# Kernel optimization log

Hardware: AMD Instinct MI355X
Metric: run time of the kernel (lower is better)

Reference implementation:

```python
import jax, jax.numpy as jnp
import numpy as np
import math

DIM = 384
HEADS = 6
HID = 32  # PositionalEncodingFourier hidden_dim
B, H, W = 16, 56, 56


def _layer_norm(x, g, b, eps=1e-6):
    mu = jnp.mean(x, axis=-1, keepdims=True)
    var = jnp.mean((x - mu) ** 2, axis=-1, keepdims=True)
    return (x - mu) * jax.lax.rsqrt(var + eps) * g + b


def _pos_encoding_fourier(Bb, Hh, Ww, w, b):
    # EdgeNeXt PositionalEncodingFourier with all-False mask: cumsum == arange+1
    scale = 2.0 * math.pi
    y_embed = jnp.arange(1, Hh + 1, dtype=jnp.float32)[:, None] / (Hh + 1e-6) * scale
    x_embed = jnp.arange(1, Ww + 1, dtype=jnp.float32)[None, :] / (Ww + 1e-6) * scale
    dim_t = 10000.0 ** (2.0 * (jnp.arange(HID) // 2).astype(jnp.float32) / HID)
    def enc(e):
        p = jnp.broadcast_to(e, (Hh, Ww))[..., None] / dim_t  # (H,W,HID)
        return jnp.stack([jnp.sin(p[..., 0::2]), jnp.cos(p[..., 1::2])], axis=-1).reshape(Hh, Ww, HID)
    pos = jnp.concatenate([enc(y_embed), enc(x_embed)], axis=-1)  # (H,W,2*HID)
    pos = pos @ w.T + b  # 1x1 conv token_projection as matmul -> (H,W,DIM)
    return jnp.broadcast_to(jnp.transpose(pos, (2, 0, 1))[None], (Bb, DIM, Hh, Ww))


def _forward(x, pos_w, pos_b, ln_g, ln_b, gamma_xca, temperature,
             qkv_w, qkv_b, proj_w, proj_b, rpb_table, conv_w,
             bn_g, bn_b, bn_mean, bn_var, gamma):
    Bb, C, Hh, Ww = x.shape
    N = Hh * Ww
    d = C // HEADS
    xt = jnp.transpose(x.reshape(Bb, C, N), (0, 2, 1))  # (B,N,C)
    pos = _pos_encoding_fourier(Bb, Hh, Ww, pos_w, pos_b)
    xt = xt + jnp.transpose(pos.reshape(Bb, C, N), (0, 2, 1))

    # relative position bias (seq_len T=2): gather (T,T,h) -> expand (h,d^2,T,T)
    # -> nearest interp x0.5 selects element (0,0) -> pixel_shuffle(d) of constant
    # channels == per-head scalar broadcast over the (d,d) channel-attention map.
    T = 2
    rel_idx = jnp.arange(T)[:, None] - jnp.arange(T)[None, :] + T - 1  # (2,2)
    rpb = rpb_table[rel_idx.reshape(-1)].reshape(T, T, HEADS)
    bias = rpb[0, 0][None, :, None, None]  # (1,heads,1,1), broadcasts over (d,d)

    # XCA: cross-covariance (channel) attention
    xn = _layer_norm(xt, ln_g, ln_b)
    qkv = (xn @ qkv_w.T + qkv_b).reshape(Bb, N, 3, HEADS, d)
    qkv = jnp.transpose(qkv, (2, 0, 3, 4, 1))  # (3,B,h,d,N)
    q, k, v = qkv[0], qkv[1], qkv[2]
    q = q / jnp.maximum(jnp.linalg.norm(q, axis=-1, keepdims=True), 1e-12)
    k = k / jnp.maximum(jnp.linalg.norm(k, axis=-1, keepdims=True), 1e-12)
    attn = jnp.einsum('bhdn,bhen->bhde', q, k) * temperature + bias  # (B,h,d,d)
    attn = jax.nn.softmax(attn, axis=-1)
    out = jnp.einsum('bhde,bhen->bhdn', attn, v)  # (B,h,d,N)
    out = jnp.transpose(out, (0, 3, 1, 2)).reshape(Bb, N, C)
    out = out @ proj_w.T + proj_b
    xt = xt + gamma_xca * out

    x2 = jnp.transpose(xt, (0, 2, 1)).reshape(Bb, C, Hh, Ww)
    # pwconv0: conv3x3 (dim->dim, expan_ration hardcoded to 1) + BN(inference) + SiLU
    xi = jax.lax.conv_general_dilated(x2, conv_w, (1, 1), [(1, 1), (1, 1)],
                                      dimension_numbers=('NCHW', 'OIHW', 'NCHW'))
    xi = (xi - bn_mean[None, :, None, None]) * jax.lax.rsqrt(bn_var + 1e-5)[None, :, None, None]
    xi = xi * bn_g[None, :, None, None] + bn_b[None, :, None, None]
    xi = xi * jax.nn.sigmoid(xi)  # SiLU
    x2 = x2 + xi

    # faithful to source: raw reshape (NOT permute) of contiguous NCHW into (B,H,W,C)
    x3 = x2.reshape(Bb, Hh, Ww, C) * gamma
    x3 = jnp.transpose(x3, (0, 3, 1, 2))
    return x + x3


def setup_inputs() -> dict:
    key = jax.random.key(0)
    ks = jax.random.split(key, 10)
    d3 = 3 * DIM
    return {
        'x': jax.random.normal(ks[0], (B, DIM, H, W), jnp.float32),
        'pos_w': jax.random.normal(ks[1], (DIM, 2 * HID), jnp.float32) * 0.05,
        'pos_b': jnp.zeros((DIM,), jnp.float32),
        'ln_g': jnp.ones((DIM,), jnp.float32),
        'ln_b': jnp.zeros((DIM,), jnp.float32),
        'gamma_xca': jax.random.normal(ks[2], (DIM,), jnp.float32) * 0.1,
        'temperature': jnp.ones((HEADS, 1, 1), jnp.float32),
        'qkv_w': jax.random.normal(ks[3], (d3, DIM), jnp.float32) * (DIM ** -0.5),
        'qkv_b': jnp.zeros((d3,), jnp.float32),
        'proj_w': jax.random.normal(ks[4], (DIM, DIM), jnp.float32) * (DIM ** -0.5),
        'proj_b': jnp.zeros((DIM,), jnp.float32),
        'rpb_table': jax.random.normal(ks[5], (3, HEADS), jnp.float32) * 0.02,
        'conv_w': jax.random.normal(ks[6], (DIM, DIM, 3, 3), jnp.float32) * 0.02,
        'bn_g': jnp.ones((DIM,), jnp.float32),
        'bn_b': jnp.zeros((DIM,), jnp.float32),
        'bn_mean': jax.random.normal(ks[7], (DIM,), jnp.float32) * 0.1,
        'bn_var': jax.random.uniform(ks[8], (DIM,), jnp.float32, 0.5, 1.5),
        'gamma': jax.random.normal(ks[9], (DIM,), jnp.float32) * 0.1,
    }


def reference(x, pos_w, pos_b, ln_g, ln_b, gamma_xca, temperature,
              qkv_w, qkv_b, proj_w, proj_b, rpb_table, conv_w,
              bn_g, bn_b, bn_mean, bn_var, gamma):
    return _forward(x, pos_w, pos_b, ln_g, ln_b, gamma_xca, temperature,
                    qkv_w, qkv_b, proj_w, proj_b, rpb_table, conv_w,
                    bn_g, bn_b, bn_mean, bn_var, gamma)
```

## Files before the change

### kernel.cpp

```cpp
#include <hip/hip_runtime.h>
#include <hip/hip_bf16.h>
#include <math.h>

#define DIM 384
#define HEADS 6
#define NN 3136
#define BB 16
#define BH (BB*HEADS)
#define HP 58
#define NP (HP*HP)

typedef __attribute__((ext_vector_type(8))) short short8;
typedef __attribute__((ext_vector_type(4))) short short4v;
typedef __attribute__((ext_vector_type(4))) float f32x4;

__device__ __forceinline__ float bf2f(unsigned short u) {
    union { unsigned int i; float f; } v; v.i = ((unsigned int)u) << 16; return v.f;
}
__device__ __forceinline__ unsigned short f2bf(float f) {
    union { float f; unsigned int i; } v; v.f = f;
    unsigned int r = v.i + 0x7fffu + ((v.i >> 16) & 1u);
    return (unsigned short)(r >> 16);
}
__device__ __forceinline__ void glds16(const unsigned short* g, void* l) {
    __builtin_amdgcn_global_load_lds(
        (const __attribute__((address_space(1))) unsigned int*)g,
        (__attribute__((address_space(3))) unsigned int*)l, 16, 0, 0);
}

__global__ void kw_convert(const float* __restrict__ qkv_w, const float* __restrict__ proj_w,
                           const float* __restrict__ conv_w,
                           unsigned short* __restrict__ Wq, unsigned short* __restrict__ Wp,
                           unsigned short* __restrict__ Wc) {
    int tid = blockIdx.x * 256 + threadIdx.x;
    int stride = gridDim.x * 256;
    for (int i = tid; i < 3*DIM*DIM; i += stride) Wq[i] = f2bf(qkv_w[i]);
    for (int i = tid; i < DIM*DIM; i += stride) Wp[i] = f2bf(proj_w[i]);
    for (int i = tid; i < DIM*DIM*9; i += stride) {
        int ii = i % DIM; int rest = i / DIM; int tap = rest % 9; int o = rest / 9;
        Wc[i] = f2bf(conv_w[(size_t)(o*DIM + ii)*9 + tap]);
    }
}

__global__ void k_pos(const float* __restrict__ pos_w, const float* __restrict__ pos_b,
                      float* __restrict__ P) {
    int n = blockIdx.x; int h = n / 56, w = n % 56;
    __shared__ float feat[64];
    int t = threadIdx.x;
    if (t < 64) {
        int axis = t >> 5;
        int k = t & 31; int i = k >> 1;
        float e = (float)((axis ? w : h) + 1) / 56.000001f * 6.28318530717958647692f;
        float arg = e / powf(10000.0f, (float)i / 16.0f);
        feat[t] = (k & 1) ? cosf(arg) : sinf(arg);
    }
    __syncthreads();
    for (int c = t; c < DIM; c += blockDim.x) {
        float s = pos_b[c];
        #pragma unroll 8
        for (int k = 0; k < 64; k++) s += feat[k] * pos_w[c*64 + k];
        P[(size_t)n*DIM + c] = s;
    }
}

__global__ __launch_bounds__(256) void k_tln(const float* __restrict__ x, const float* __restrict__ P,
                                             const float* __restrict__ g, const float* __restrict__ be,
                                             unsigned short* __restrict__ XTb, unsigned short* __restrict__ XN) {
    __shared__ float tile[32][388];
    int blk = blockIdx.x;
    int b = blk / 98, nt = blk % 98;
    int n0 = nt*32;
    int t = threadIdx.x;
    #pragma unroll
    for (int it = 0; it < 12; it++) {
        int task = it*256 + t;
        int c = task >> 3, seg = task & 7;
        float4 v = *reinterpret_cast<const float4*>(x + ((size_t)(b*DIM + c))*NN + n0 + seg*4);
        tile[seg*4+0][c] = v.x; tile[seg*4+1][c] = v.y;
        tile[seg*4+2][c] = v.z; tile[seg*4+3][c] = v.w;
    }
    __syncthreads();
    int row = t >> 3, sub = t & 7;
    int n = n0 + row;
    f32x4 xp[12];
    float s = 0.f;
    #pragma unroll
    for (int k = 0; k < 12; k++) {
        int c0 = (k*8 + sub)*4;
        float4 tv = *reinterpret_cast<float4*>(&tile[row][c0]);
        float4 pv = *reinterpret_cast<const float4*>(P + (size_t)n*DIM + c0);
        f32x4 xv = {tv.x+pv.x, tv.y+pv.y, tv.z+pv.z, tv.w+pv.w};
        xp[k] = xv;
        s += xv[0]+xv[1]+xv[2]+xv[3];
        unsigned short pkx[4];
        #pragma unroll
        for (int e=0;e<4;e++) pkx[e] = f2bf(xv[e]);
        *reinterpret_cast<short4v*>(XTb + ((size_t)(b*NN + n))*DIM + c0) = *(short4v*)pkx;
    }
    s += __shfl_xor(s, 1, 64); s += __shfl_xor(s, 2, 64); s += __shfl_xor(s, 4, 64);
    float mean = s * (1.0f/384.0f);
    float sq = 0.f;
    #pragma unroll
    for (int k = 0; k < 12; k++) {
        #pragma unroll
        for (int e = 0; e < 4; e++) { float d = xp[k][e]-mean; sq += d*d; }
    }
    sq += __shfl_xor(sq, 1, 64); sq += __shfl_xor(sq, 2, 64); sq += __shfl_xor(sq, 4, 64);
    float rs = rsqrtf(sq * (1.0f/384.0f) + 1e-6f);
    #pragma unroll
    for (int k = 0; k < 12; k++) {
        int c0 = (k*8 + sub)*4;
        unsigned short pk[4];
        #pragma unroll
        for (int e = 0; e < 4; e++)
            pk[e] = f2bf((xp[k][e]-mean)*rs*g[c0+e] + be[c0+e]);
        *reinterpret_cast<short4v*>(XN + ((size_t)(b*NN + n))*DIM + c0) = *(short4v*)pk;
    }
}

template<int MODE>
__global__ __launch_bounds__(256) void k_gemm(
    const unsigned short* __restrict__ A, const unsigned short* __restrict__ Wt,
    const float* __restrict__ bias,
    unsigned short* __restrict__ Qb, unsigned short* __restrict__ Kb, unsigned short* __restrict__ Vt,
    const unsigned short* __restrict__ XTb, const float* __restrict__ gxca, unsigned short* __restrict__ X2p)
{
    __shared__ __align__(16) char smem[35328];
    auto ctA = (float(*)[69])smem;
    auto ctB = (float(*)[130])smem;

    constexpr int NCT = (MODE == 0) ? 9 : 3;
    constexpr int CPX = (MODE == 0) ? 441 : 147;
    int bid = blockIdx.x;
    int orig = (bid & 7)*CPX + (bid >> 3);
    int ct = orig % NCT, mt = orig / NCT;
    int m0 = mt*128, o0 = ct*128;
    int t = threadIdx.x;
    int wave = t >> 6, lane = t & 63;
    int wr = wave >> 1, wc = wave & 1;
    int lr = lane & 15, lg = lane >> 4;

    int r0 = t >> 2;
    int swcol = (((t & 3) ^ ((t >> 3) & 3)) << 3);
    const unsigned short* a0 = A  + (size_t)(m0 + r0)*384 + swcol;
    const unsigned short* a1 = A  + (size_t)(m0 + 64 + r0)*384 + swcol;
    const unsigned short* b0 = Wt + (size_t)(o0 + r0)*384 + swcol;
    const unsigned short* b1 = Wt + (size_t)(o0 + 64 + r0)*384 + swcol;
    int rsw = ((lr >> 1) & 3) << 3;

    auto stage = [&](char* base, int c) {
        glds16(a0 + c, base + wave*1024);
        glds16(a1 + c, base + 4096 + wave*1024);
        glds16(b0 + c, base + 8192 + wave*1024);
        glds16(b1 + c, base + 12288 + wave*1024);
    };

    f32x4 acc[4][4];
    #pragma unroll
    for (int i=0;i<4;i++) for (int j=0;j<4;j++) acc[i][j] = (f32x4){0.f,0.f,0.f,0.f};

    stage(smem, 0);
    for (int kk = 0; kk < 12; kk++) {
        if (kk < 11) {
            stage(smem + ((kk+1)&1)*16384, (kk+1)*32);
            asm volatile("s_waitcnt vmcnt(4)" ::: "memory");
        } else {
            asm volatile("s_waitcnt vmcnt(0)" ::: "memory");
        }
        __builtin_amdgcn_s_barrier();
        __builtin_amdgcn_sched_barrier(0);
        auto As = (unsigned short(*)[32])(smem + (kk&1)*16384);
        auto Bs = (unsigned short(*)[32])(smem + (kk&1)*16384 + 8192);
        short8 af[4], bfv[4];
        #pragma unroll
        for (int i=0;i<4;i++) af[i]  = *(short8*)&As[wr*64 + i*16 + lr][(lg*8) ^ rsw];
        #pragma unroll
        for (int j=0;j<4;j++) bfv[j] = *(short8*)&Bs[wc*64 + j*16 + lr][(lg*8) ^ rsw];
        #pragma unroll
        for (int i=0;i<4;i++)
            #pragma unroll
            for (int j=0;j<4;j++)
                acc[i][j] = __builtin_amdgcn_mfma_f32_16x16x32_bf16(af[i], bfv[j], acc[i][j], 0, 0, 0);
        __builtin_amdgcn_s_barrier();
        __builtin_amdgcn_sched_barrier(0);
    }

    int comp = (MODE == 0) ? (o0 / DIM) : 0;
    for (int mh = 0; mh < 2; mh++) {
        __syncthreads();
        bool useB = (MODE == 1) || (MODE == 0 && comp == 2);
        if (wr == mh) {
            if (useB) {
                #pragma unroll
                for (int i=0;i<4;i++) for (int j=0;j<4;j++) for (int r=0;r<4;r++)
                    ctB[i*16 + lg*4 + r][wc*64 + j*16 + lr] = acc[i][j][r];
            } else {
                #pragma unroll
                for (int i=0;i<4;i++) for (int j=0;j<4;j++) for (int r=0;r<4;r++)
                    ctA[wc*64 + j*16 + lr][i*16 + lg*4 + r] = acc[i][j][r];
            }
        }
        __syncthreads();
        if (MODE == 1) {
            for (int q = t; q < 1024; q += 256) {
                int row = q >> 4, seg = q & 15;
                int m = m0 + mh*64 + row; int b = m/NN; int n = m - b*NN;
                int py = n/56, px = n - py*56;
                int og0 = o0 + seg*8;
                short8 xvb = *(const short8*)(XTb + (size_t)m*DIM + og0);
                unsigned short pk[8];
                #pragma unroll
                for (int e=0;e<8;e++) {
                    float val = ctB[row][seg*8+e] + bias[og0+e];
                    pk[e] = f2bf(bf2f((unsigned short)xvb[e]) + gxca[og0+e]*val);
                }
                *(short8*)(X2p + ((size_t)(b*NP + (py+1)*HP + px + 1))*DIM + og0) = *(short8*)pk;
            }
        } else if (comp < 2) {
            unsigned short* Dst = (comp == 0) ? Qb : Kb;
            for (int q = t; q < 2048; q += 256) {
                int row = q >> 4, seg = q & 15;
                int og = o0 + row; int rem = og - comp*DIM;
                int hh = rem >> 6, dd = rem & 63;
                int m4 = m0 + mh*64 + seg*4; int b = m4/NN; int n = m4 - b*NN;
                float bv = bias[og];
                unsigned short pk[4];
                #pragma unroll
                for (int e=0;e<4;e++) pk[e] = f2bf(ctA[row][seg*4+e] + bv);
                *(short4v*)(Dst + ((size_t)((b*HEADS + hh)*64 + dd))*NN + n) = *(short4v*)pk;
            }
        } else {
            for (int q = t; q < 1024; q += 256) {
                int row = q >> 4, seg = q & 15;
                int m = m0 + mh*64 + row; int b = m/NN; int n = m - b*NN;
                int og0 = o0 + seg*8; int rem0 = og0 - 2*DIM;
                int hh = rem0 >> 6, dd0 = rem0 & 63;
                unsigned short pk[8];
                #pragma unroll
                for (int e=0;e<8;e++) pk[e] = f2bf(ctB[row][seg*8+e] + bias[og0+e]);
                *(short8*)(Vt + ((size_t)((b*HEADS + hh)*NN + n))*64 + dd0) = *(short8*)pk;
            }
        }
    }
}

__global__ __launch_bounds__(256) void k_pad(unsigned short* __restrict__ X2p) {
    int b = blockIdx.x, part = blockIdx.y;
    unsigned short* base = X2p + (size_t)b*NP*DIM;
    short8 z = {0,0,0,0,0,0,0,0};
    for (int task = part*256 + threadIdx.x; task < 10944; task += 2048) {
        int pos = task / 48, seg = task - pos*48;
        int py, px;
        if (pos < 58)       { py = 0;  px = pos; }
        else if (pos < 116) { py = 57; px = pos - 58; }
        else if (pos < 172) { py = pos - 115; px = 0; }
        else                { py = pos - 171; px = 57; }
        *(short8*)(base + ((size_t)(py*HP + px))*DIM + seg*8) = z;
    }
}

__global__ __launch_bounds__(256, 3) void k_conv(
    const unsigned short* __restrict__ A, const unsigned short* __restrict__ Wt,
    const float* __restrict__ bn_g, const float* __restrict__ bn_b,
    const float* __restrict__ bn_mean, const float* __restrict__ bn_var,
    unsigned short* __restrict__ Yout)
{
    __shared__ __align__(16) char smem[49152];
    auto ctA = (float(*)[69])smem;
    auto X2s = (unsigned short(*)[68])(smem + 17664);

    int bid = blockIdx.x;
    int orig = (bid & 7)*150 + (bid >> 3);
    int ct = orig % 3; int rest = orig / 3;
    int tile = rest % 25; int b = rest / 25;
    int n0 = tile*128, o0 = ct*128;
    int t = threadIdx.x;
    int wave = t >> 6, lane = t & 63;
    int wr = wave >> 1, wc = wave & 1;
    int lr = lane & 15, lg = lane >> 4;
    int qb = n0 + 2*(n0/56);
    const size_t bbase = (size_t)b*NP*DIM;

    int swcol = (((t & 3) ^ ((t >> 3) & 3)) << 3);
    const unsigned short* asrc[4];
    #pragma unroll
    for (int j=0;j<4;j++) {
        int task = j*256 + t;
        int row = task >> 2;
        int q = qb + row; if (q > NP-1) q = NP-1;
        asrc[j] = A + bbase + (size_t)q*DIM + swcol;
    }
    const unsigned short* bsrc0 = Wt + (size_t)(o0 + (t>>2))*3456 + swcol;
    const unsigned short* bsrc1 = Wt + (size_t)(o0 + 64 + (t>>2))*3456 + swcol;

    int qrel[4];
    #pragma unroll
    for (int i=0;i<4;i++) {
        int loc = wr*64 + i*16 + lr;
        int n = n0 + loc; if (n >= NN) n = NN-1;
        qrel[i] = n + 2*(n/56) - qb;
    }

    auto stageA = [&](int bufsel, int c) {
        #pragma unroll
        for (int j=0;j<4;j++) glds16(asrc[j] + c, smem + bufsel*16384 + j*4096 + wave*1024);
    };
    auto stageB = [&](int slot, int off) {
        glds16(bsrc0 + off, smem + 32768 + slot*8192 + wave*1024);
        glds16(bsrc1 + off, smem + 32768 + slot*8192 + 4096 + wave*1024);
    };

    f32x4 acc[4][4];
    #pragma unroll
    for (int i=0;i<4;i++) for (int j=0;j<4;j++) acc[i][j] = (f32x4){0.f,0.f,0.f,0.f};

    stageA(0, 0); stageB(0, 0);
    for (int kk = 0; kk < 12; kk++) {
        auto Ah = (unsigned short(*)[32])(smem + (kk&1)*16384);
        #pragma unroll
        for (int tap = 0; tap < 9; tap++) {
            if (kk < 11 || tap < 8) {
                int off = (tap < 8) ? ((tap+1)*384 + kk*32) : ((kk+1)*32);
                stageB((kk+tap+1)&1, off);
            }
            if (tap == 6 && kk < 11) stageA((kk+1)&1, (kk+1)*32);
            if (kk < 11 && (tap == 6 || tap == 7))
                asm volatile("s_waitcnt vmcnt(6)" ::: "memory");
            else if (kk == 11 && tap == 8)
                asm volatile("s_waitcnt vmcnt(0)" ::: "memory");
            else
                asm volatile("s_waitcnt vmcnt(2)" ::: "memory");
            __builtin_amdgcn_s_barrier();
            __builtin_amdgcn_sched_barrier(0);
            auto Bs = (unsigned short(*)[32])(smem + 32768 + ((kk+tap)&1)*8192);
            int toff = (tap/3)*58 + (tap%3);
            short8 af[4], bfv[4];
            #pragma unroll
            for (int j=0;j<4;j++) {
                int brow = wc*64 + j*16 + lr;
                bfv[j] = *(short8*)&Bs[brow][(lg*8) ^ (((brow>>1)&3)<<3)];
            }
            #pragma unroll
            for (int i=0;i<4;i++) {
                int row = qrel[i] + toff;
                af[i] = *(short8*)&Ah[row][(lg*8) ^ (((row>>1)&3)<<3)];
            }
            #pragma unroll
            for (int i=0;i<4;i++)
                #pragma unroll
                for (int j=0;j<4;j++)
                    acc[i][j] = __builtin_amdgcn_mfma_f32_16x16x32_bf16(af[i], bfv[j], acc[i][j], 0, 0, 0);
            __builtin_amdgcn_s_barrier();
            __builtin_amdgcn_sched_barrier(0);
        }
    }

    for (int mh = 0; mh < 2; mh++) {
        for (int oh = 0; oh < 2; oh++) {
            __syncthreads();
            if (wr == mh && wc == oh) {
                #pragma unroll
                for (int i=0;i<4;i++) for (int j=0;j<4;j++) for (int r=0;r<4;r++)
                    ctA[j*16 + lr][i*16 + lg*4 + r] = acc[i][j][r];
            }
            for (int q = t; q < 512; q += 256) {
                int row = q >> 3, sg = q & 7;
                int n = n0 + mh*64 + row; int nc = (n < NN) ? n : NN-1;
                int qq = nc + 2*(nc/56) + 59;
                short8 v = *(const short8*)(A + bbase + (size_t)qq*DIM + o0 + oh*64 + sg*8);
                short4v lo = {v[0],v[1],v[2],v[3]}, hi = {v[4],v[5],v[6],v[7]};
                *(short4v*)&X2s[row][sg*8]     = lo;
                *(short4v*)&X2s[row][sg*8 + 4] = hi;
            }
            __syncthreads();
            for (int q = t; q < 512; q += 256) {
                int orow = q >> 3, sg = q & 7;
                int o = o0 + oh*64 + orow;
                int n = n0 + mh*64 + sg*8;
                if (n < NN) {
                    float mean = bn_mean[o], rs = rsqrtf(bn_var[o] + 1e-5f);
                    float gg = bn_g[o], bb2 = bn_b[o];
                    unsigned short pk[8];
                    #pragma unroll
                    for (int e=0;e<8;e++) {
                        float xi = (ctA[orow][sg*8+e] - mean)*rs*gg + bb2;
                        float si = xi / (1.0f + __expf(-xi));
                        pk[e] = f2bf(si + bf2f(X2s[sg*8+e][orow]));
                    }
                    *(short8*)(Yout + ((size_t)(b*DIM + o))*NN + n) = *(short8*)pk;
                }
            }
        }
    }
}

__global__ __launch_bounds__(256) void k_qk(const unsigned short* __restrict__ Qb,
                                            const unsigned short* __restrict__ Kb,
                                            float* __restrict__ Gp, float* __restrict__ Np) {
    int cx = blockIdx.x, bh = blockIdx.y;
    int t = threadIdx.x, wave = t >> 6, lane = t & 63;
    int lr = lane & 15, lg = lane >> 4;
    {
        int row = t >> 1, p = t & 1;
        const unsigned short* src = (row < 64)
            ? Qb + ((size_t)bh*64 + row)*NN + cx*448
            : Kb + ((size_t)bh*64 + (row-64))*NN + cx*448;
        float s = 0.f;
        #pragma unroll
        for (int it = 0; it < 28; it++) {
            short8 v = *(const short8*)(src + p*224 + it*8);
            #pragma unroll
            for (int jj=0;jj<8;jj++) { float f = bf2f((unsigned short)v[jj]); s += f*f; }
        }
        s += __shfl_xor(s, 1, 64);
        if (p == 0) Np[((size_t)bh*7 + cx)*128 + row] = s;
    }
    f32x4 acc[4];
    #pragma unroll
    for (int j=0;j<4;j++) acc[j] = (f32x4){0.f,0.f,0.f,0.f};
    const unsigned short* qrow = Qb + ((size_t)bh*64 + wave*16 + lr)*NN + cx*448;
    const unsigned short* kbase = Kb + (size_t)bh*64*NN + cx*448;
    for (int ks = 0; ks < 14; ks++) {
        short8 a = *(const short8*)(qrow + ks*32 + lg*8);
        #pragma unroll
        for (int j=0;j<4;j++) {
            short8 bfr = *(const short8*)(kbase + (size_t)(j*16+lr)*NN + ks*32 + lg*8);
            acc[j] = __builtin_amdgcn_mfma_f32_16x16x32_bf16(a, bfr, acc[j], 0, 0, 0);
        }
    }
    float* gbase = Gp + ((size_t)bh*7 + cx)*4096;
    #pragma unroll
    for (int j=0;j<4;j++)
        #pragma unroll
        for (int r=0;r<4;r++)
            gbase[(wave*16 + lg*4 + r)*64 + j*16 + lr] = acc[j][r];
}

__global__ __launch_bounds__(256) void k_sm(const float* __restrict__ Gp, const float* __restrict__ Np,
                                            const float* __restrict__ temperature,
                                            const float* __restrict__ rpb,
                                            unsigned short* __restrict__ ATT) {
    int bh = blockIdx.x; int h = bh % HEADS;
    int t = threadIdx.x;
    __shared__ float snorm[128];
    if (t < 128) {
        float s = 0.f;
        #pragma unroll
        for (int cx=0;cx<7;cx++) s += Np[((size_t)bh*7 + cx)*128 + t];
        snorm[t] = fmaxf(sqrtf(s), 1e-12f);
    }
    __syncthreads();
    int dq = t >> 2, de0 = (t & 3) * 16;
    f32x4 g[4];
    #pragma unroll
    for (int i=0;i<4;i++) g[i] = (f32x4){0.f,0.f,0.f,0.f};
    #pragma unroll
    for (int cx=0;cx<7;cx++) {
        const float* base = Gp + ((size_t)bh*7 + cx)*4096 + dq*64 + de0;
        #pragma unroll
        for (int i=0;i<4;i++) {
            float4 v = *(const float4*)(base + i*4);
            g[i][0]+=v.x; g[i][1]+=v.y; g[i][2]+=v.z; g[i][3]+=v.w;
        }
    }
    float temp = temperature[h];
    float bias = rpb[HEADS + h];
    float qn = snorm[dq];
    float lv[16]; float mx = -1e30f;
    #pragma unroll
    for (int i=0;i<4;i++)
        #pragma unroll
        for (int e=0;e<4;e++) {
            int de = de0 + i*4 + e;
            float v = g[i][e] / (qn * snorm[64 + de]) * temp + bias;
            lv[i*4+e] = v; mx = fmaxf(mx, v);
        }
    mx = fmaxf(mx, __shfl_xor(mx, 1, 64));
    mx = fmaxf(mx, __shfl_xor(mx, 2, 64));
    float se = 0.f;
    #pragma unroll
    for (int e=0;e<16;e++) { lv[e] = __expf(lv[e]-mx); se += lv[e]; }
    se += __shfl_xor(se, 1, 64);
    se += __shfl_xor(se, 2, 64);
    float inv = 1.0f/se;
    unsigned short pk[16];
    #pragma unroll
    for (int e=0;e<16;e++) pk[e] = f2bf(lv[e]*inv);
    unsigned short* dst = ATT + ((size_t)bh*64 + dq)*64 + de0;
    *(short8*)dst       = *(short8*)pk;
    *(short8*)(dst + 8) = *(short8*)(pk + 8);
}

__global__ __launch_bounds__(256) void k_pv(const unsigned short* __restrict__ ATT,
                                            const unsigned short* __restrict__ Vt,
                                            unsigned short* __restrict__ XCA) {
    int nt = blockIdx.x, bh = blockIdx.y;
    int b = bh / HEADS, h = bh % HEADS;
    int t = threadIdx.x, wave = t >> 6, lane = t & 63;
    int lr = lane & 15, lg = lane >> 4;
    int n0 = nt*64;
    __shared__ float ctP[64][67];
    f32x4 acc[4];
    for (int i=0;i<4;i++) acc[i] = (f32x4){0.f,0.f,0.f,0.f};
    for (int ks=0; ks<2; ks++) {
        short8 bfr = *reinterpret_cast<const short8*>(Vt + ((size_t)bh*NN + n0 + wave*16 + lr)*64 + ks*32 + lg*8);
        for (int i=0;i<4;i++) {
            short8 a = *reinterpret_cast<const short8*>(ATT + ((size_t)bh*64 + i*16 + lr)*64 + ks*32 + lg*8);
            acc[i] = __builtin_amdgcn_mfma_f32_16x16x32_bf16(a, bfr, acc[i], 0, 0, 0);
        }
    }
    int nl = wave*16 + lr;
    #pragma unroll
    for (int i=0;i<4;i++)
        #pragma unroll
        for (int r=0;r<4;r++) ctP[nl][i*16 + lg*4 + r] = acc[i][r];
    __syncthreads();
    for (int q = t; q < 512; q += 256) {
        int row = q >> 3, seg = q & 7;
        unsigned short pk[8];
        #pragma unroll
        for (int e=0;e<8;e++) pk[e] = f2bf(ctP[row][seg*8+e]);
        *(short8*)(XCA + ((size_t)(b*NN + n0 + row))*DIM + h*64 + seg*8) = *(short8*)pk;
    }
}

__global__ __launch_bounds__(256) void k_final(const float* __restrict__ x, const unsigned short* __restrict__ Yb,
                                               const float* __restrict__ gamma, float* __restrict__ out) {
    int i = blockIdx.x, b = blockIdx.y, kc = blockIdx.z;
    __shared__ float tile[56*193];
    int t = threadIdx.x;
    int k0 = kc*192;
    const unsigned short* ybase = Yb + (size_t)b*DIM*NN + (size_t)i*21504 + k0;
    for (int q = t; q < 56*24; q += 256) {
        int j = q / 24, c8 = (q % 24) * 8;
        short8 v = *(const short8*)(ybase + (size_t)j*384 + c8);
        float* dst = &tile[j*193 + c8];
        #pragma unroll
        for (int e=0;e<8;e++) dst[e] = bf2f((unsigned short)v[e]);
    }
    __syncthreads();
    for (int q = t; q < 192*56; q += 256) {
        int kl = q / 56, j = q % 56;
        int k = k0 + kl;
        size_t gi = ((size_t)(b*DIM + k))*NN + (size_t)i*56 + j;
        out[gi] = x[gi] + gamma[k] * tile[j*193 + kl];
    }
}

extern "C" void kernel_launch(void* const* d_in, const int* in_sizes, int n_in,
                              void* d_out, int out_size, void* d_ws, size_t ws_size,
                              hipStream_t stream) {
    const float* x       = (const float*)d_in[0];
    const float* pos_w   = (const float*)d_in[1];
    const float* pos_b   = (const float*)d_in[2];
    const float* ln_g    = (const float*)d_in[3];
    const float* ln_b    = (const float*)d_in[4];
    const float* gxca    = (const float*)d_in[5];
    const float* temp    = (const float*)d_in[6];
    const float* qkv_w   = (const float*)d_in[7];
    const float* qkv_b   = (const float*)d_in[8];
    const float* proj_w  = (const float*)d_in[9];
    const float* proj_b  = (const float*)d_in[10];
    const float* rpb     = (const float*)d_in[11];
    const float* conv_w  = (const float*)d_in[12];
    const float* bn_g    = (const float*)d_in[13];
    const float* bn_b    = (const float*)d_in[14];
    const float* bn_mean = (const float*)d_in[15];
    const float* bn_var  = (const float*)d_in[16];
    const float* gamma   = (const float*)d_in[17];
    float* out = (float*)d_out;
    char* ws = (char*)d_ws;

    const size_t oP   = 0;
    const size_t oXT  = oP   + 4816896;
    const size_t oXN  = oXT  + 77070336;
    const size_t oQ   = oXN  + 38535168;
    const size_t oK   = oQ   + 38535168;
    const size_t oV   = oK   + 38535168;
    const size_t oATT = oV   + 38535168;
    const size_t oWq  = oATT + 786432;
    const size_t oWp  = oWq  + 884736;
    const size_t oWc  = oWp  + 294912;

    float* P            = (float*)(ws + oP);
    unsigned short* XTb = (unsigned short*)(ws + oXT);
    unsigned short* Yb  = (unsigned short*)(ws + oXT);
    unsigned short* XN  = (unsigned short*)(ws + oXN);
    float* Gp           = (float*)(ws + oXN);
    float* Np           = (float*)(ws + oXN + 11010048);
    unsigned short* XCA = (unsigned short*)(ws + oXN);
    unsigned short* Qb  = (unsigned short*)(ws + oQ);
    unsigned short* X2p = (unsigned short*)(ws + oQ);
    unsigned short* Kb  = (unsigned short*)(ws + oK);
    unsigned short* Vt  = (unsigned short*)(ws + oV);
    unsigned short* ATT = (unsigned short*)(ws + oATT);
    unsigned short* Wq  = (unsigned short*)(ws + oWq);
    unsigned short* Wp  = (unsigned short*)(ws + oWp);
    unsigned short* Wc  = (unsigned short*)(ws + oWc);

    kw_convert<<<256, 256, 0, stream>>>(qkv_w, proj_w, conv_w, Wq, Wp, Wc);
    k_pos<<<NN, 128, 0, stream>>>(pos_w, pos_b, P);
    k_tln<<<BB*98, 256, 0, stream>>>(x, P, ln_g, ln_b, XTb, XN);
    k_gemm<0><<<3528, 256, 0, stream>>>(XN, Wq, qkv_b,
        Qb, Kb, Vt, nullptr, nullptr, nullptr);
    k_qk<<<dim3(7, BH), 256, 0, stream>>>(Qb, Kb, Gp, Np);
    k_sm<<<BH, 256, 0, stream>>>(Gp, Np, temp, rpb, ATT);
    k_pad<<<dim3(BB, 8), 256, 0, stream>>>(X2p);
    k_pv<<<dim3(49, BH), 256, 0, stream>>>(ATT, Vt, XCA);
    k_gemm<1><<<1176, 256, 0, stream>>>(XCA, Wp, proj_b,
        nullptr, nullptr, nullptr, XTb, gxca, X2p);
    k_conv<<<1200, 256, 0, stream>>>(X2p, Wc, bn_g, bn_b, bn_mean, bn_var, Yb);
    k_final<<<dim3(56, BB, 2), 256, 0, stream>>>(x, Yb, gamma, out);
}
```

Baseline: 459.8 us.

## Load conv weights directly into registers and merge small setup kernels

The conv kernel stops staging weight tiles through LDS and loads each wave's B fragments straight from global memory into double-buffered registers. This removes the per-tap barriers and halves the LDS footprint, so each k-step needs only one barrier. The loop is unrolled by two so the register buffer index stays static. The weight-conversion and positional-encoding kernels are merged into one launch, and the padding zero-fill moves into the softmax kernel, cutting two launches. In exchange the weights are read from global or L2 once per wave instead of once per block, and register pressure goes up.

```diff
diff --git a/kernel.cpp b/kernel.cpp
--- a/kernel.cpp
+++ b/kernel.cpp
@@ -28,38 +28,38 @@
         (__attribute__((address_space(3))) unsigned int*)l, 16, 0, 0);
 }
 
-__global__ void kw_convert(const float* __restrict__ qkv_w, const float* __restrict__ proj_w,
-                           const float* __restrict__ conv_w,
-                           unsigned short* __restrict__ Wq, unsigned short* __restrict__ Wp,
-                           unsigned short* __restrict__ Wc) {
-    int tid = blockIdx.x * 256 + threadIdx.x;
-    int stride = gridDim.x * 256;
-    for (int i = tid; i < 3*DIM*DIM; i += stride) Wq[i] = f2bf(qkv_w[i]);
-    for (int i = tid; i < DIM*DIM; i += stride) Wp[i] = f2bf(proj_w[i]);
-    for (int i = tid; i < DIM*DIM*9; i += stride) {
-        int ii = i % DIM; int rest = i / DIM; int tap = rest % 9; int o = rest / 9;
-        Wc[i] = f2bf(conv_w[(size_t)(o*DIM + ii)*9 + tap]);
-    }
-}
-
-__global__ void k_pos(const float* __restrict__ pos_w, const float* __restrict__ pos_b,
-                      float* __restrict__ P) {
-    int n = blockIdx.x; int h = n / 56, w = n % 56;
-    __shared__ float feat[64];
+__global__ void k_prep(const float* __restrict__ qkv_w, const float* __restrict__ proj_w,
+                       const float* __restrict__ conv_w,
+                       const float* __restrict__ pos_w, const float* __restrict__ pos_b,
+                       unsigned short* __restrict__ Wq, unsigned short* __restrict__ Wp,
+                       unsigned short* __restrict__ Wc, float* __restrict__ P) {
     int t = threadIdx.x;
-    if (t < 64) {
-        int axis = t >> 5;
-        int k = t & 31; int i = k >> 1;
-        float e = (float)((axis ? w : h) + 1) / 56.000001f * 6.28318530717958647692f;
-        float arg = e / powf(10000.0f, (float)i / 16.0f);
-        feat[t] = (k & 1) ? cosf(arg) : sinf(arg);
-    }
-    __syncthreads();
-    for (int c = t; c < DIM; c += blockDim.x) {
-        float s = pos_b[c];
-        #pragma unroll 8
-        for (int k = 0; k < 64; k++) s += feat[k] * pos_w[c*64 + k];
-        P[(size_t)n*DIM + c] = s;
+    if (blockIdx.x < NN) {
+        int n = blockIdx.x; int h = n / 56, w = n % 56;
+        __shared__ float feat[64];
+        if (t < 64) {
+            int axis = t >> 5;
+            int k = t & 31; int i = k >> 1;
+            float e = (float)((axis ? w : h) + 1) / 56.000001f * 6.28318530717958647692f;
+            float arg = e / powf(10000.0f, (float)i / 16.0f);
+            feat[t] = (k & 1) ? cosf(arg) : sinf(arg);
+        }
+        __syncthreads();
+        for (int c = t; c < DIM; c += 256) {
+            float s = pos_b[c];
+            #pragma unroll 8
+            for (int k = 0; k < 64; k++) s += feat[k] * pos_w[c*64 + k];
+            P[(size_t)n*DIM + c] = s;
+        }
+    } else {
+        int tid = (blockIdx.x - NN) * 256 + t;
+        int stride = 256 * 256;
+        for (int i = tid; i < 3*DIM*DIM; i += stride) Wq[i] = f2bf(qkv_w[i]);
+        for (int i = tid; i < DIM*DIM; i += stride) Wp[i] = f2bf(proj_w[i]);
+        for (int i = tid; i < DIM*DIM*9; i += stride) {
+            int ii = i % DIM; int rest = i / DIM; int tap = rest % 9; int o = rest / 9;
+            Wc[i] = f2bf(conv_w[(size_t)(o*DIM + ii)*9 + tap]);
+        }
     }
 }
 
@@ -244,20 +244,39 @@
     }
 }
 
-__global__ __launch_bounds__(256) void k_pad(unsigned short* __restrict__ X2p) {
-    int b = blockIdx.x, part = blockIdx.y;
-    unsigned short* base = X2p + (size_t)b*NP*DIM;
-    short8 z = {0,0,0,0,0,0,0,0};
-    for (int task = part*256 + threadIdx.x; task < 10944; task += 2048) {
-        int pos = task / 48, seg = task - pos*48;
-        int py, px;
-        if (pos < 58)       { py = 0;  px = pos; }
-        else if (pos < 116) { py = 57; px = pos - 58; }
-        else if (pos < 172) { py = pos - 115; px = 0; }
-        else                { py = pos - 171; px = 57; }
-        *(short8*)(base + ((size_t)(py*HP + px))*DIM + seg*8) = z;
-    }
-}
+#define CONV_KK(KK, PAR)                                                                   \
+  {                                                                                        \
+    auto Ah = (unsigned short(*)[32])(smem + ((KK)&1)*16384);                              \
+    _Pragma("unroll")                                                                      \
+    for (int tap = 0; tap < 9; tap++) {                                                    \
+      if (tap < 8) {                                                                       \
+        _Pragma("unroll")                                                                  \
+        for (int j=0;j<4;j++)                                                              \
+          breg[(tap+PAR+1)&1][j] = *(const short8*)(bptr[j] + (tap+1)*384 + (KK)*32);      \
+      } else if ((KK) < 11) {                                                              \
+        _Pragma("unroll")                                                                  \
+        for (int j=0;j<4;j++)                                                              \
+          breg[(tap+PAR+1)&1][j] = *(const short8*)(bptr[j] + ((KK)+1)*32);                \
+      }                                                                                    \
+      if (tap == 6 && (KK) < 11) stageA(((KK)+1)&1, ((KK)+1)*32);                          \
+      int toff = (tap/3)*58 + (tap%3);                                                     \
+      short8 af[4];                                                                        \
+      _Pragma("unroll")                                                                    \
+      for (int i=0;i<4;i++) {                                                              \
+        int row = qrel[i] + toff;                                                          \
+        af[i] = *(short8*)&Ah[row][(lg*8) ^ (((row>>1)&3)<<3)];                            \
+      }                                                                                    \
+      _Pragma("unroll")                                                                    \
+      for (int i=0;i<4;i++)                                                                \
+        _Pragma("unroll")                                                                  \
+        for (int j=0;j<4;j++)                                                              \
+          acc[i][j] = __builtin_amdgcn_mfma_f32_16x16x32_bf16(af[i],                       \
+                        breg[(tap+PAR)&1][j], acc[i][j], 0, 0, 0);                         \
+    }                                                                                      \
+    asm volatile("s_waitcnt vmcnt(4)" ::: "memory");                                       \
+    __builtin_amdgcn_s_barrier();                                                          \
+    __builtin_amdgcn_sched_barrier(0);                                                     \
+  }
 
 __global__ __launch_bounds__(256, 3) void k_conv(
     const unsigned short* __restrict__ A, const unsigned short* __restrict__ Wt,
@@ -265,7 +284,7 @@
     const float* __restrict__ bn_mean, const float* __restrict__ bn_var,
     unsigned short* __restrict__ Yout)
 {
-    __shared__ __align__(16) char smem[49152];
+    __shared__ __align__(16) char smem[32768];
     auto ctA = (float(*)[69])smem;
     auto X2s = (unsigned short(*)[68])(smem + 17664);
 
@@ -290,8 +309,9 @@
         int q = qb + row; if (q > NP-1) q = NP-1;
         asrc[j] = A + bbase + (size_t)q*DIM + swcol;
     }
-    const unsigned short* bsrc0 = Wt + (size_t)(o0 + (t>>2))*3456 + swcol;
-    const unsigned short* bsrc1 = Wt + (size_t)(o0 + 64 + (t>>2))*3456 + swcol;
+    const unsigned short* bptr[4];
+    #pragma unroll
+    for (int j=0;j<4;j++) bptr[j] = Wt + (size_t)(o0 + wc*64 + j*16 + lr)*3456 + lg*8;
 
     int qrel[4];
     #pragma unroll
@@ -305,54 +325,24 @@
         #pragma unroll
         for (int j=0;j<4;j++) glds16(asrc[j] + c, smem + bufsel*16384 + j*4096 + wave*1024);
     };
-    auto stageB = [&](int slot, int off) {
-        glds16(bsrc0 + off, smem + 32768 + slot*8192 + wave*1024);
-        glds16(bsrc1 + off, smem + 32768 + slot*8192 + 4096 + wave*1024);
-    };
 
     f32x4 acc[4][4];
     #pragma unroll
     for (int i=0;i<4;i++) for (int j=0;j<4;j++) acc[i][j] = (f32x4){0.f,0.f,0.f,0.f};
-
-    stageA(0, 0); stageB(0, 0);
-    for (int kk = 0; kk < 12; kk++) {
-        auto Ah = (unsigned short(*)[32])(smem + (kk&1)*16384);
-        #pragma unroll
-        for (int tap = 0; tap < 9; tap++) {
-            if (kk < 11 || tap < 8) {
-                int off = (tap < 8) ? ((tap+1)*384 + kk*32) : ((kk+1)*32);
-                stageB((kk+tap+1)&1, off);
-            }
-            if (tap == 6 && kk < 11) stageA((kk+1)&1, (kk+1)*32);
-            if (kk < 11 && (tap == 6 || tap == 7))
-                asm volatile("s_waitcnt vmcnt(6)" ::: "memory");
-            else if (kk == 11 && tap == 8)
-                asm volatile("s_waitcnt vmcnt(0)" ::: "memory");
-            else
-                asm volatile("s_waitcnt vmcnt(2)" ::: "memory");
-            __builtin_amdgcn_s_barrier();
-            __builtin_amdgcn_sched_barrier(0);
-            auto Bs = (unsigned short(*)[32])(smem + 32768 + ((kk+tap)&1)*8192);
-            int toff = (tap/3)*58 + (tap%3);
-            short8 af[4], bfv[4];
-            #pragma unroll
-            for (int j=0;j<4;j++) {
-                int brow = wc*64 + j*16 + lr;
-                bfv[j] = *(short8*)&Bs[brow][(lg*8) ^ (((brow>>1)&3)<<3)];
-            }
-            #pragma unroll
-            for (int i=0;i<4;i++) {
-                int row = qrel[i] + toff;
-                af[i] = *(short8*)&Ah[row][(lg*8) ^ (((row>>1)&3)<<3)];
-            }
-            #pragma unroll
-            for (int i=0;i<4;i++)
-                #pragma unroll
-                for (int j=0;j<4;j++)
-                    acc[i][j] = __builtin_amdgcn_mfma_f32_16x16x32_bf16(af[i], bfv[j], acc[i][j], 0, 0, 0);
-            __builtin_amdgcn_s_barrier();
-            __builtin_amdgcn_sched_barrier(0);
-        }
+    short8 breg[2][4];
+
+    stageA(0, 0);
+    #pragma unroll
+    for (int j=0;j<4;j++) breg[0][j] = *(const short8*)(bptr[j]);
+    asm volatile("s_waitcnt vmcnt(0)" ::: "memory");
+    __builtin_amdgcn_s_barrier();
+    __builtin_amdgcn_sched_barrier(0);
+
+    for (int kkp = 0; kkp < 6; kkp++) {
+        int kk = kkp*2;
+        CONV_KK(kk, 0);
+        kk = kkp*2 + 1;
+        CONV_KK(kk, 1);
     }
 
     for (int mh = 0; mh < 2; mh++) {
@@ -439,7 +429,8 @@
 __global__ __launch_bounds__(256) void k_sm(const float* __restrict__ Gp, const float* __restrict__ Np,
                                             const float* __restrict__ temperature,
                                             const float* __restrict__ rpb,
-                                            unsigned short* __restrict__ ATT) {
+                                            unsigned short* __restrict__ ATT,
+                                            unsigned short* __restrict__ X2p) {
     int bh = blockIdx.x; int h = bh % HEADS;
     int t = threadIdx.x;
     __shared__ float snorm[128];
@@ -489,6 +480,19 @@
     unsigned short* dst = ATT + ((size_t)bh*64 + dq)*64 + de0;
     *(short8*)dst       = *(short8*)pk;
     *(short8*)(dst + 8) = *(short8*)(pk + 8);
+
+    int pb = bh / 6, part = bh % 6;
+    unsigned short* base2 = X2p + (size_t)pb*NP*DIM;
+    short8 z = {0,0,0,0,0,0,0,0};
+    for (int task = part*256 + t; task < 10944; task += 1536) {
+        int pos = task / 48, seg = task - pos*48;
+        int py, px;
+        if (pos < 58)       { py = 0;  px = pos; }
+        else if (pos < 116) { py = 57; px = pos - 58; }
+        else if (pos < 172) { py = pos - 115; px = 0; }
+        else                { py = pos - 171; px = 57; }
+        *(short8*)(base2 + ((size_t)(py*HP + px))*DIM + seg*8) = z;
+    }
 }
 
 __global__ __launch_bounds__(256) void k_pv(const unsigned short* __restrict__ ATT,
@@ -598,14 +602,12 @@
     unsigned short* Wp  = (unsigned short*)(ws + oWp);
     unsigned short* Wc  = (unsigned short*)(ws + oWc);
 
-    kw_convert<<<256, 256, 0, stream>>>(qkv_w, proj_w, conv_w, Wq, Wp, Wc);
-    k_pos<<<NN, 128, 0, stream>>>(pos_w, pos_b, P);
+    k_prep<<<NN + 256, 256, 0, stream>>>(qkv_w, proj_w, conv_w, pos_w, pos_b, Wq, Wp, Wc, P);
     k_tln<<<BB*98, 256, 0, stream>>>(x, P, ln_g, ln_b, XTb, XN);
     k_gemm<0><<<3528, 256, 0, stream>>>(XN, Wq, qkv_b,
         Qb, Kb, Vt, nullptr, nullptr, nullptr);
     k_qk<<<dim3(7, BH), 256, 0, stream>>>(Qb, Kb, Gp, Np);
-    k_sm<<<BH, 256, 0, stream>>>(Gp, Np, temp, rpb, ATT);
-    k_pad<<<dim3(BB, 8), 256, 0, stream>>>(X2p);
+    k_sm<<<BH, 256, 0, stream>>>(Gp, Np, temp, rpb, ATT, X2p);
     k_pv<<<dim3(49, BH), 256, 0, stream>>>(ATT, Vt, XCA);
     k_gemm<1><<<1176, 256, 0, stream>>>(XCA, Wp, proj_b,
         nullptr, nullptr, nullptr, XTb, gxca, X2p);
```

Measured after the change: 625.6 us. +36.1%, slower.
